# Optimization experiments

Measured on AMD Instinct MI355X. Metric: run time of the kernel, lower is better.

## Reference

```python
import jax, jax.numpy as jnp
import numpy as np

D_MODEL = 1024
N_HEADS = 16
HEAD_DIM = D_MODEL // N_HEADS
B, S = 4, 2048


def setup_inputs() -> dict:
    key = jax.random.key(0)
    ks = jax.random.split(key, 12)
    scale = 1.0 / np.sqrt(D_MODEL)
    inp = {
        "query": jax.random.normal(ks[0], (B, S, D_MODEL), dtype=jnp.float32),
        "key": jax.random.normal(ks[1], (B, S, D_MODEL), dtype=jnp.float32),
        "value": jax.random.normal(ks[2], (B, S, D_MODEL), dtype=jnp.float32),
        "mask": jnp.ones((B, 1, S), dtype=jnp.int32),
        "Wq": jax.random.normal(ks[3], (D_MODEL, D_MODEL), dtype=jnp.float32) * scale,
        "bq": jnp.zeros((D_MODEL,), dtype=jnp.float32),
        "Wk": jax.random.normal(ks[4], (D_MODEL, D_MODEL), dtype=jnp.float32) * scale,
        "bk": jnp.zeros((D_MODEL,), dtype=jnp.float32),
        "Wv": jax.random.normal(ks[5], (D_MODEL, D_MODEL), dtype=jnp.float32) * scale,
        "bv": jnp.zeros((D_MODEL,), dtype=jnp.float32),
        "Wo": jax.random.normal(ks[6], (D_MODEL, D_MODEL), dtype=jnp.float32) * scale,
        "bo": jnp.zeros((D_MODEL,), dtype=jnp.float32),
    }
    return inp


def reference(query, key, value, mask, Wq, bq, Wk, bk, Wv, bv, Wo, bo):
    bsz = query.shape[0]
    # Linear projections (torch nn.Linear: x @ W.T + b), split into heads -> [b, h, s, d]
    def proj(x, W, b):
        y = jnp.einsum("bse,de->bsd", x, W) + b
        return y.reshape(bsz, -1, N_HEADS, HEAD_DIM).transpose(0, 2, 1, 3)

    q = proj(query, Wq, bq)
    k = proj(key, Wk, bk)
    v = proj(value, Wv, bv)

    # NOTE: faithful to source — scale by 1/sqrt(d_model), not 1/sqrt(head_dim)
    scores = jnp.einsum("bhqd,bhkd->bhqk", q, k) / jnp.sqrt(jnp.asarray(D_MODEL, q.dtype))
    # mask [b, 1, s_k] -> unsqueeze(1) -> [b, 1, 1, s_k]; fill -inf where mask == 0
    m = mask[:, None, :, :]
    scores = jnp.where(m == 0, jnp.asarray(-jnp.inf, scores.dtype), scores)
    p_attn = jax.nn.softmax(scores, axis=-1)
    ctx = jnp.einsum("bhqk,bhkd->bhqd", p_attn, v)

    concat = ctx.transpose(0, 2, 1, 3).reshape(bsz, -1, D_MODEL)
    out = jnp.einsum("bse,de->bsd", concat, Wo) + bo
    return out
```

## Files before the change

### kernel.cpp

```cpp
#include <hip/hip_runtime.h>
#include <hip/hip_bf16.h>

typedef unsigned short u16;
typedef __attribute__((ext_vector_type(4))) short short4v;
typedef __attribute__((ext_vector_type(8))) short short8;
typedef __attribute__((ext_vector_type(4))) float float4v;

__device__ __forceinline__ void async_copy16(const void* g, void* l) {
  __builtin_amdgcn_global_load_lds(
      (const __attribute__((address_space(1))) unsigned int*)g,
      (__attribute__((address_space(3))) unsigned int*)l,
      16, 0, 0);
}

__device__ __forceinline__ u16 f2bf(float f) {
  __hip_bfloat16 h = __float2bfloat16(f);
  return *reinterpret_cast<u16*>(&h);
}

struct CArgs {
  const float* in[7];
  u16* out[7];
  int n[7];
};

__global__ void conv_bf16(CArgs a) {
  int t = blockIdx.y;
  int n = a.n[t];
  long i = ((long)blockIdx.x * blockDim.x + threadIdx.x) * 8;
  if (i >= n) return;
  const float4v* f = (const float4v*)(a.in[t] + i);
  float4v lo = f[0], hi = f[1];
  u16 o[8];
  o[0] = f2bf(lo.x); o[1] = f2bf(lo.y); o[2] = f2bf(lo.z); o[3] = f2bf(lo.w);
  o[4] = f2bf(hi.x); o[5] = f2bf(hi.y); o[6] = f2bf(hi.z); o[7] = f2bf(hi.w);
  *(short8*)(a.out[t] + i) = *(const short8*)o;
}

template <bool OUT_F32>
__global__ __launch_bounds__(256, 2)
void gemm_bt(const u16* __restrict__ A, const u16* __restrict__ W,
             const float* __restrict__ bias, void* __restrict__ Cp,
             int M, int N, int K, int mode) {
  __shared__ __attribute__((aligned(16))) u16 As[128 * 32];
  __shared__ __attribute__((aligned(16))) u16 Ws[128 * 32];

  const int tid  = threadIdx.x;
  const int lane = tid & 63;
  const int wave = tid >> 6;
  const int ln15 = lane & 15;
  const int quad = lane >> 4;
  const int m0 = blockIdx.y * 128;
  const int n0 = blockIdx.x * 128;
  const int wm = (wave & 1) * 64;
  const int wn = (wave >> 1) * 64;

  float4v acc[4][4];
#pragma unroll
  for (int i = 0; i < 4; i++)
#pragma unroll
    for (int j = 0; j < 4; j++) acc[i][j] = (float4v)0.0f;

  for (int k0 = 0; k0 < K; k0 += 32) {
#pragma unroll
    for (int c = 0; c < 2; c++) {
      int e = (c * 256 + tid) * 8;
      int r = e >> 5, col = e & 31;
      async_copy16(A + (size_t)(m0 + r) * K + k0 + col, (void*)(As + e));
      async_copy16(W + (size_t)(n0 + r) * K + k0 + col, (void*)(Ws + e));
    }
    __syncthreads();

    short8 af[4], bfr[4];
#pragma unroll
    for (int i = 0; i < 4; i++)
      af[i] = *(const short8*)(As + (wm + i * 16 + ln15) * 32 + quad * 8);
#pragma unroll
    for (int j = 0; j < 4; j++)
      bfr[j] = *(const short8*)(Ws + (wn + j * 16 + ln15) * 32 + quad * 8);
#pragma unroll
    for (int i = 0; i < 4; i++)
#pragma unroll
      for (int j = 0; j < 4; j++)
        acc[i][j] = __builtin_amdgcn_mfma_f32_16x16x32_bf16(af[i], bfr[j], acc[i][j], 0, 0, 0);
    __syncthreads();
  }

#pragma unroll
  for (int j = 0; j < 4; j++) {
    int n = n0 + wn + j * 16 + ln15;
    float bval = bias[n];
#pragma unroll
    for (int i = 0; i < 4; i++) {
#pragma unroll
      for (int r = 0; r < 4; r++) {
        int m = m0 + wm + i * 16 + quad * 4 + r;
        float v = acc[i][j][r] + bval;
        size_t addr;
        if (mode == 0) {
          addr = (size_t)m * N + n;
        } else {
          int b = m >> 11, s = m & 2047;
          int h = n >> 6, dh = n & 63;
          if (mode == 1) addr = (((size_t)(b * 16 + h)) * 2048 + s) * 64 + dh;
          else           addr = (((size_t)(b * 16 + h)) * 64 + dh) * 2048 + s;
        }
        if (OUT_F32) ((float*)Cp)[addr] = v;
        else         ((u16*)Cp)[addr] = f2bf(v);
      }
    }
  }
}

#define QP 72
__global__ __launch_bounds__(256, 2)
void attn(const u16* __restrict__ Q, const u16* __restrict__ K,
          const u16* __restrict__ Vt, const int* __restrict__ mask,
          u16* __restrict__ Ct) {
  __shared__ __attribute__((aligned(16))) u16 Qs[128 * QP];
  __shared__ __attribute__((aligned(16))) u16 Ks[2][64 * QP];
  __shared__ __attribute__((aligned(16))) u16 Vs[2][64 * QP];
  __shared__ __attribute__((aligned(16))) u16 Ps[128 * QP];

  const int tid  = threadIdx.x;
  const int lane = tid & 63;
  const int wave = tid >> 6;
  const int ln15 = lane & 15;
  const int quad = lane >> 4;
  const int bh = blockIdx.y;
  const int b = bh >> 4, h = bh & 15;
  const int q0 = blockIdx.x * 128;
  const int qr0 = wave * 32;

  const u16* Qg = Q + ((size_t)bh * 2048 + q0) * 64;
  const u16* Kg = K + (size_t)bh * 2048 * 64;
  const u16* Vg = Vt + (size_t)bh * 64 * 2048;

#pragma unroll
  for (int c = 0; c < 4; c++) {
    int e = (c * 256 + tid) * 8;
    int r = e >> 6, col = e & 63;
    *(short8*)(Qs + r * QP + col) = *(const short8*)(Qg + e);
  }
#pragma unroll
  for (int c = 0; c < 2; c++) {
    int e = (c * 256 + tid) * 8;
    int r = e >> 6, col = e & 63;
    *(short8*)(Ks[0] + r * QP + col) = *(const short8*)(Kg + (size_t)r * 64 + col);
    *(short8*)(Vs[0] + r * QP + col) = *(const short8*)(Vg + (size_t)r * 2048 + col);
  }

  float4v acc_o[2][4];
#pragma unroll
  for (int i = 0; i < 2; i++)
#pragma unroll
    for (int j = 0; j < 4; j++) acc_o[i][j] = (float4v)0.0f;
  float lrow[2][4];
#pragma unroll
  for (int i = 0; i < 2; i++)
#pragma unroll
    for (int r = 0; r < 4; r++) lrow[i][r] = 0.0f;

  for (int t = 0; t < 32; t++) {
    const int buf = t & 1;
    __syncthreads();

    short8 kreg[2], vreg[2];
    const bool havenext = (t + 1) < 32;
    if (havenext) {
      int kt2 = (t + 1) * 64;
#pragma unroll
      for (int c = 0; c < 2; c++) {
        int e = (c * 256 + tid) * 8;
        int r = e >> 6, col = e & 63;
        kreg[c] = *(const short8*)(Kg + (size_t)(kt2 + r) * 64 + col);
        vreg[c] = *(const short8*)(Vg + (size_t)r * 2048 + kt2 + col);
      }
    }

    float4v sacc[2][4];
#pragma unroll
    for (int i = 0; i < 2; i++)
#pragma unroll
      for (int j = 0; j < 4; j++) sacc[i][j] = (float4v)0.0f;
#pragma unroll
    for (int kk = 0; kk < 64; kk += 32) {
      short8 af[2], bfr[4];
#pragma unroll
      for (int i = 0; i < 2; i++)
        af[i] = *(const short8*)(Qs + (qr0 + i * 16 + ln15) * QP + kk + quad * 8);
#pragma unroll
      for (int j = 0; j < 4; j++)
        bfr[j] = *(const short8*)(Ks[buf] + (j * 16 + ln15) * QP + kk + quad * 8);
#pragma unroll
      for (int i = 0; i < 2; i++)
#pragma unroll
        for (int j = 0; j < 4; j++)
          sacc[i][j] = __builtin_amdgcn_mfma_f32_16x16x32_bf16(af[i], bfr[j], sacc[i][j], 0, 0, 0);
    }

    float mb[4];
#pragma unroll
    for (int j = 0; j < 4; j++)
      mb[j] = (mask[b * 2048 + t * 64 + j * 16 + ln15] == 0) ? -1e30f : 0.0f;

#pragma unroll
    for (int i = 0; i < 2; i++) {
#pragma unroll
      for (int r = 0; r < 4; r++) {
        int prow = (qr0 + i * 16 + quad * 4 + r) * QP;
        float sum = 0.0f;
#pragma unroll
        for (int j = 0; j < 4; j++) {
          float p = __expf(sacc[i][j][r] * 0.03125f + mb[j]);
          sum += p;
          Ps[prow + j * 16 + ln15] = f2bf(p);
        }
        lrow[i][r] += sum;
      }
    }

    if (havenext) {
#pragma unroll
      for (int c = 0; c < 2; c++) {
        int e = (c * 256 + tid) * 8;
        int r = e >> 6, col = e & 63;
        *(short8*)(Ks[buf ^ 1] + r * QP + col) = kreg[c];
        *(short8*)(Vs[buf ^ 1] + r * QP + col) = vreg[c];
      }
    }

#pragma unroll
    for (int kk = 0; kk < 64; kk += 32) {
      short8 af[2], bfr[4];
#pragma unroll
      for (int i = 0; i < 2; i++)
        af[i] = *(const short8*)(Ps + (qr0 + i * 16 + ln15) * QP + kk + quad * 8);
#pragma unroll
      for (int jd = 0; jd < 4; jd++)
        bfr[jd] = *(const short8*)(Vs[buf] + (jd * 16 + ln15) * QP + kk + quad * 8);
#pragma unroll
      for (int i = 0; i < 2; i++)
#pragma unroll
        for (int jd = 0; jd < 4; jd++)
          acc_o[i][jd] = __builtin_amdgcn_mfma_f32_16x16x32_bf16(af[i], bfr[jd], acc_o[i][jd], 0, 0, 0);
    }
  }

#pragma unroll
  for (int i = 0; i < 2; i++) {
#pragma unroll
    for (int r = 0; r < 4; r++) {
      float l = lrow[i][r];
      l += __shfl_xor(l, 1);
      l += __shfl_xor(l, 2);
      l += __shfl_xor(l, 4);
      l += __shfl_xor(l, 8);
      float inv = 1.0f / l;
      int s = q0 + qr0 + i * 16 + quad * 4 + r;
#pragma unroll
      for (int jd = 0; jd < 4; jd++) {
        float v = acc_o[i][jd][r] * inv;
        Ct[((size_t)(b * 2048 + s)) * 1024 + h * 64 + jd * 16 + ln15] = f2bf(v);
      }
    }
  }
}


extern "C" void kernel_launch(void* const* d_in, const int* in_sizes, int n_in,
                              void* d_out, int out_size, void* d_ws, size_t ws_size,
                              hipStream_t stream) {
  int iq, ik, iv, im, iWq, ibq, iWk, ibk, iWv, ibv, iWo, ibo;
  if (in_sizes[0] == 8388608) {
    iq = 0; ik = 1; iv = 2; im = 3;
    iWq = 4; ibq = 5; iWk = 6; ibk = 7; iWv = 8; ibv = 9; iWo = 10; ibo = 11;
  } else {
    iWk = 0; iWo = 1; iWq = 2; iWv = 3;
    ibk = 4; ibo = 5; ibq = 6; ibv = 7;
    ik = 8; im = 9; iq = 10; iv = 11;
  }
  const float* query = (const float*)d_in[iq];
  const float* key   = (const float*)d_in[ik];
  const float* value = (const float*)d_in[iv];
  const int*   mask  = (const int*)d_in[im];
  const float* Wq = (const float*)d_in[iWq];
  const float* bq = (const float*)d_in[ibq];
  const float* Wk = (const float*)d_in[iWk];
  const float* bk = (const float*)d_in[ibk];
  const float* Wv = (const float*)d_in[iWv];
  const float* bv = (const float*)d_in[ibv];
  const float* Wo = (const float*)d_in[iWo];
  const float* bo = (const float*)d_in[ibo];

  const long U  = 8388608;
  const long Wn = 1048576;
  u16* ws = (u16*)d_ws;
  u16* cq   = ws;
  u16* ck   = cq + U;
  u16* cv   = ck + U;
  u16* cWq  = cv + U;
  u16* cWk  = cWq + Wn;
  u16* cWv  = cWk + Wn;
  u16* cWo  = cWv + Wn;
  u16* qws  = cWo + Wn;
  u16* kws  = qws + U;
  u16* vtws = cq;
  u16* cws  = ck;

  dim3 blk(256);

  CArgs ca;
  ca.in[0] = query; ca.out[0] = cq;  ca.n[0] = (int)U;
  ca.in[1] = key;   ca.out[1] = ck;  ca.n[1] = (int)U;
  ca.in[2] = value; ca.out[2] = cv;  ca.n[2] = (int)U;
  ca.in[3] = Wq;    ca.out[3] = cWq; ca.n[3] = (int)Wn;
  ca.in[4] = Wk;    ca.out[4] = cWk; ca.n[4] = (int)Wn;
  ca.in[5] = Wv;    ca.out[5] = cWv; ca.n[5] = (int)Wn;
  ca.in[6] = Wo;    ca.out[6] = cWo; ca.n[6] = (int)Wn;
  conv_bf16<<<dim3(4096, 7), blk, 0, stream>>>(ca);

  dim3 gproj(8, 64);
  gemm_bt<false><<<gproj, blk, 0, stream>>>(cq, cWq, bq, qws, 8192, 1024, 1024, 1);
  gemm_bt<false><<<gproj, blk, 0, stream>>>(ck, cWk, bk, kws, 8192, 1024, 1024, 1);
  gemm_bt<false><<<gproj, blk, 0, stream>>>(cv, cWv, bv, vtws, 8192, 1024, 1024, 2);
  attn<<<dim3(16, 64), blk, 0, stream>>>(qws, kws, vtws, mask, cws);
  gemm_bt<true><<<gproj, blk, 0, stream>>>(cws, cWo, bo, d_out, 8192, 1024, 1024, 0);
}
```

Measured before the change: 446.7 us.

## Keep Q fragments in registers, shrink LDS, raise attention occupancy to three blocks

Q tiles now load straight from global memory into per-wave register fragments, which removes the Q shared-memory buffer and its LDS reads on every tile. The P buffer uses a narrower 68-element pitch and is read back as two 4-element loads, and launch bounds move to 3 blocks per CU so the smaller LDS footprint allows more resident blocks. The exponent becomes exp2f with a folded log2(e)/32 constant, and the bf16 conversion becomes a plain truncation instead of round-to-nearest. The cost is higher register pressure under the tighter bound and slightly less precise P values.

New measurement: 487.4 us. +9.1%, slower.

```diff
diff --git a/kernel.cpp b/kernel.cpp
--- a/kernel.cpp
+++ b/kernel.cpp
@@ -112,15 +112,15 @@
   }
 }
 
-#define QP 72
-__global__ __launch_bounds__(256, 2)
+#define KVP 72
+#define PSP 68
+__global__ __launch_bounds__(256, 3)
 void attn(const u16* __restrict__ Q, const u16* __restrict__ K,
           const u16* __restrict__ Vt, const int* __restrict__ mask,
           u16* __restrict__ Ct) {
-  __shared__ __attribute__((aligned(16))) u16 Qs[128 * QP];
-  __shared__ __attribute__((aligned(16))) u16 Ks[2][64 * QP];
-  __shared__ __attribute__((aligned(16))) u16 Vs[2][64 * QP];
-  __shared__ __attribute__((aligned(16))) u16 Ps[128 * QP];
+  __shared__ __attribute__((aligned(16))) u16 Ks[2][64 * KVP];
+  __shared__ __attribute__((aligned(16))) u16 Vs[2][64 * KVP];
+  __shared__ __attribute__((aligned(16))) u16 Ps[128 * PSP];
 
   const int tid  = threadIdx.x;
   const int lane = tid & 63;
@@ -132,22 +132,24 @@
   const int q0 = blockIdx.x * 128;
   const int qr0 = wave * 32;
 
-  const u16* Qg = Q + ((size_t)bh * 2048 + q0) * 64;
   const u16* Kg = K + (size_t)bh * 2048 * 64;
   const u16* Vg = Vt + (size_t)bh * 64 * 2048;
 
-#pragma unroll
-  for (int c = 0; c < 4; c++) {
-    int e = (c * 256 + tid) * 8;
-    int r = e >> 6, col = e & 63;
-    *(short8*)(Qs + r * QP + col) = *(const short8*)(Qg + e);
-  }
+  short8 qf[2][2];
+#pragma unroll
+  for (int i = 0; i < 2; i++) {
+    const u16* qrow = Q + ((size_t)bh * 2048 + q0 + qr0 + i * 16 + ln15) * 64;
+#pragma unroll
+    for (int k2 = 0; k2 < 2; k2++)
+      qf[i][k2] = *(const short8*)(qrow + k2 * 32 + quad * 8);
+  }
+
 #pragma unroll
   for (int c = 0; c < 2; c++) {
     int e = (c * 256 + tid) * 8;
     int r = e >> 6, col = e & 63;
-    *(short8*)(Ks[0] + r * QP + col) = *(const short8*)(Kg + (size_t)r * 64 + col);
-    *(short8*)(Vs[0] + r * QP + col) = *(const short8*)(Vg + (size_t)r * 2048 + col);
+    *(short8*)(Ks[0] + r * KVP + col) = *(const short8*)(Kg + (size_t)r * 64 + col);
+    *(short8*)(Vs[0] + r * KVP + col) = *(const short8*)(Vg + (size_t)r * 2048 + col);
   }
 
   float4v acc_o[2][4];
@@ -160,6 +162,8 @@
   for (int i = 0; i < 2; i++)
 #pragma unroll
     for (int r = 0; r < 4; r++) lrow[i][r] = 0.0f;
+
+  const float CE = 0.04508422f;
 
   for (int t = 0; t < 32; t++) {
     const int buf = t & 1;
@@ -178,43 +182,40 @@
       }
     }
 
-    float4v sacc[2][4];
-#pragma unroll
-    for (int i = 0; i < 2; i++)
-#pragma unroll
-      for (int j = 0; j < 4; j++) sacc[i][j] = (float4v)0.0f;
-#pragma unroll
-    for (int kk = 0; kk < 64; kk += 32) {
-      short8 af[2], bfr[4];
-#pragma unroll
-      for (int i = 0; i < 2; i++)
-        af[i] = *(const short8*)(Qs + (qr0 + i * 16 + ln15) * QP + kk + quad * 8);
-#pragma unroll
-      for (int j = 0; j < 4; j++)
-        bfr[j] = *(const short8*)(Ks[buf] + (j * 16 + ln15) * QP + kk + quad * 8);
-#pragma unroll
-      for (int i = 0; i < 2; i++)
-#pragma unroll
-        for (int j = 0; j < 4; j++)
-          sacc[i][j] = __builtin_amdgcn_mfma_f32_16x16x32_bf16(af[i], bfr[j], sacc[i][j], 0, 0, 0);
-    }
-
     float mb[4];
 #pragma unroll
     for (int j = 0; j < 4; j++)
       mb[j] = (mask[b * 2048 + t * 64 + j * 16 + ln15] == 0) ? -1e30f : 0.0f;
 
+    float4v sacc[2][4];
+#pragma unroll
+    for (int i = 0; i < 2; i++)
+#pragma unroll
+      for (int j = 0; j < 4; j++) sacc[i][j] = (float4v)0.0f;
+#pragma unroll
+    for (int k2 = 0; k2 < 2; k2++) {
+      short8 bfr[4];
+#pragma unroll
+      for (int j = 0; j < 4; j++)
+        bfr[j] = *(const short8*)(Ks[buf] + (j * 16 + ln15) * KVP + k2 * 32 + quad * 8);
+#pragma unroll
+      for (int i = 0; i < 2; i++)
+#pragma unroll
+        for (int j = 0; j < 4; j++)
+          sacc[i][j] = __builtin_amdgcn_mfma_f32_16x16x32_bf16(qf[i][k2], bfr[j], sacc[i][j], 0, 0, 0);
+    }
+
 #pragma unroll
     for (int i = 0; i < 2; i++) {
 #pragma unroll
       for (int r = 0; r < 4; r++) {
-        int prow = (qr0 + i * 16 + quad * 4 + r) * QP;
+        int prow = (qr0 + i * 16 + quad * 4 + r) * PSP;
         float sum = 0.0f;
 #pragma unroll
         for (int j = 0; j < 4; j++) {
-          float p = __expf(sacc[i][j][r] * 0.03125f + mb[j]);
+          float p = exp2f(sacc[i][j][r] * CE + mb[j]);
           sum += p;
-          Ps[prow + j * 16 + ln15] = f2bf(p);
+          Ps[prow + j * 16 + ln15] = (u16)(__float_as_uint(p) >> 16);
         }
         lrow[i][r] += sum;
       }
@@ -225,8 +226,8 @@
       for (int c = 0; c < 2; c++) {
         int e = (c * 256 + tid) * 8;
         int r = e >> 6, col = e & 63;
-        *(short8*)(Ks[buf ^ 1] + r * QP + col) = kreg[c];
-        *(short8*)(Vs[buf ^ 1] + r * QP + col) = vreg[c];
+        *(short8*)(Ks[buf ^ 1] + r * KVP + col) = kreg[c];
+        *(short8*)(Vs[buf ^ 1] + r * KVP + col) = vreg[c];
       }
     }
 
@@ -234,11 +235,15 @@
     for (int kk = 0; kk < 64; kk += 32) {
       short8 af[2], bfr[4];
 #pragma unroll
-      for (int i = 0; i < 2; i++)
-        af[i] = *(const short8*)(Ps + (qr0 + i * 16 + ln15) * QP + kk + quad * 8);
+      for (int i = 0; i < 2; i++) {
+        const u16* p = Ps + (qr0 + i * 16 + ln15) * PSP + kk + quad * 8;
+        short4v lo = *(const short4v*)p;
+        short4v hi = *(const short4v*)(p + 4);
+        af[i] = __builtin_shufflevector(lo, hi, 0, 1, 2, 3, 4, 5, 6, 7);
+      }
 #pragma unroll
       for (int jd = 0; jd < 4; jd++)
-        bfr[jd] = *(const short8*)(Vs[buf] + (jd * 16 + ln15) * QP + kk + quad * 8);
+        bfr[jd] = *(const short8*)(Vs[buf] + (jd * 16 + ln15) * KVP + kk + quad * 8);
 #pragma unroll
       for (int i = 0; i < 2; i++)
 #pragma unroll
```
